# Optimization experiments

Hardware: AMD Instinct MI355X
Metric: run time of the kernel (lower is better)

## Reference

```python
import jax, jax.numpy as jnp
import numpy as np


def setup_inputs() -> dict:
    key = jax.random.key(0)
    k1, k2 = jax.random.split(key)
    N, K, E = 65536, 8, 64  # tokens, top_k, num_experts
    top_scores = jax.random.normal(k1, (N, K), dtype=jnp.float32)
    selected_experts_indices = jax.random.randint(k2, (N, K), 0, E, dtype=jnp.int32)
    return {
        "top_scores": top_scores,
        "selected_experts_indices": selected_experts_indices,
        "num_experts": E,
        "top_k": K,
    }


def reference(top_scores, selected_experts_indices, num_experts, top_k):
    # Flatten (token, slot) assignments: total = N * top_k
    expert_flat = selected_experts_indices.reshape(-1)

    # Histogram: number of assignments per expert (float32, matching torch impl)
    num_tokens_per_expert = jax.ops.segment_sum(
        jnp.ones_like(expert_flat, dtype=jnp.float32),
        expert_flat,
        num_segments=num_experts,
    )

    # Stable sort by expert id == counting sort: for each output slot, which
    # flattened assignment index lands there. Identical to the torch
    # scatter/cumsum counting-sort since both are stable.
    token_indices_experts_sorted = jnp.argsort(expert_flat, stable=True)

    # Gather routing scores into expert-sorted order
    top_scores_experts_sorted = top_scores.reshape(-1)[token_indices_experts_sorted]

    # Map flattened assignment index back to token index
    token_indices_experts_sorted = token_indices_experts_sorted // top_k

    return (top_scores_experts_sorted, token_indices_experts_sorted, num_tokens_per_expert)
```

## Files before the change

### kernel.cpp

```cpp
#include <hip/hip_runtime.h>

#define TOTAL   524288
#define NEXP    64
#define TOPK    8
#define GSIZE   256
#define BLOCK   256
#define NWAVE   4
#define CHUNK   (TOTAL / GSIZE)
#define WCHUNK  (CHUNK / NWAVE)
#define WROUNDS (WCHUNK / 64)

__global__ __launch_bounds__(BLOCK) void hist_kernel(const int* __restrict__ idx,
                                                     int* __restrict__ counts) {
    __shared__ int hist[NWAVE][NEXP];
    const int tid = threadIdx.x, lane = tid & 63, wave = tid >> 6;
    hist[wave][lane] = 0;
    const int base = blockIdx.x * CHUNK + wave * WCHUNK;
#pragma unroll
    for (int r = 0; r < WROUNDS; r++) {
        const int e = idx[base + r * 64 + lane];
        unsigned long long m = ~0ULL;
#pragma unroll
        for (int bit = 0; bit < 6; bit++) {
            const unsigned long long bb = __ballot((e >> bit) & 1);
            m &= ((e >> bit) & 1) ? bb : ~bb;
        }
        const int leader = __ffsll((long long)m) - 1;
        if (lane == leader) hist[wave][e] += __popcll(m);
    }
    __syncthreads();
    if (tid < NEXP)
        counts[blockIdx.x * NEXP + tid] =
            hist[0][tid] + hist[1][tid] + hist[2][tid] + hist[3][tid];
}

__global__ __launch_bounds__(BLOCK) void scatter_kernel(
        const float* __restrict__ scores,
        const int*   __restrict__ idx,
        const int*   __restrict__ counts,
        float*       __restrict__ out_scores,
        float*       __restrict__ out_tok,
        float*       __restrict__ out_cnt) {
    __shared__ int hist[NWAVE][NEXP];
    __shared__ int part_pre[NWAVE][NEXP];
    __shared__ int part_tot[NWAVE][NEXP];
    __shared__ int exscan_pre[NEXP];
    __shared__ int exoff[NWAVE][NEXP];
    __shared__ int run[NWAVE][NEXP];

    const int tid = threadIdx.x, lane = tid & 63, wave = tid >> 6, b = blockIdx.x;
    const unsigned long long ltmask = (1ULL << lane) - 1ULL;

    int pre = 0, tot = 0;
    {
        const int bb0 = wave * (GSIZE / NWAVE);
#pragma unroll 16
        for (int q = 0; q < GSIZE / NWAVE; q++) {
            const int bb = bb0 + q;
            const int c  = counts[bb * NEXP + lane];
            tot += c;
            pre += (bb < b) ? c : 0;
        }
    }
    part_pre[wave][lane] = pre;
    part_tot[wave][lane] = tot;

    hist[wave][lane] = 0;
    run[wave][lane]  = 0;
    const int base = b * CHUNK + wave * WCHUNK;
    int                myE[WROUNDS];
    float              myS[WROUNDS];
    unsigned long long myM[WROUNDS];
#pragma unroll
    for (int r = 0; r < WROUNDS; r++) {
        const int i = base + r * 64 + lane;
        const int e = idx[i];
        myE[r] = e;
        myS[r] = scores[i];
        unsigned long long m = ~0ULL;
#pragma unroll
        for (int bit = 0; bit < 6; bit++) {
            const unsigned long long bb = __ballot((e >> bit) & 1);
            m &= ((e >> bit) & 1) ? bb : ~bb;
        }
        myM[r] = m;
        const int leader = __ffsll((long long)m) - 1;
        if (lane == leader) hist[wave][e] += __popcll(m);
    }
    __syncthreads();

    if (wave == 0) {
        const int p = part_pre[0][lane] + part_pre[1][lane] +
                      part_pre[2][lane] + part_pre[3][lane];
        const int t = part_tot[0][lane] + part_tot[1][lane] +
                      part_tot[2][lane] + part_tot[3][lane];
        if (b == 0) out_cnt[lane] = (float)t;
        int inc = t;
#pragma unroll
        for (int d = 1; d < 64; d <<= 1) {
            const int v = __shfl_up(inc, d, 64);
            if (lane >= d) inc += v;
        }
        exscan_pre[lane] = (inc - t) + p;
    }
    __syncthreads();

    {
        int off = exscan_pre[lane];
        for (int w = 0; w < wave; w++) off += hist[w][lane];
        exoff[wave][lane] = off;
    }
    __syncthreads();

#pragma unroll
    for (int r = 0; r < WROUNDS; r++) {
        const int e = myE[r];
        const unsigned long long m = myM[r];
        const int inwave = __popcll(m & ltmask);
        const int rn     = run[wave][e];
        const int pos    = exoff[wave][e] + rn + inwave;
        out_scores[pos] = myS[r];
        out_tok[pos]    = (float)((base + r * 64 + lane) >> 3);
        __builtin_amdgcn_wave_barrier();
        const int leader = __ffsll((long long)m) - 1;
        if (lane == leader) run[wave][e] = rn + __popcll(m);
        __builtin_amdgcn_wave_barrier();
    }
}

extern "C" void kernel_launch(void* const* d_in, const int* in_sizes, int n_in,
                              void* d_out, int out_size, void* d_ws, size_t ws_size,
                              hipStream_t stream) {
    const float* top_scores = (const float*)d_in[0];
    const int*   sel_idx    = (const int*)d_in[1];
    float*       out        = (float*)d_out;
    int*         counts     = (int*)d_ws;

    float* out_scores = out;
    float* out_tok    = out + TOTAL;
    float* out_cnt    = out + 2 * TOTAL;

    hist_kernel<<<GSIZE, BLOCK, 0, stream>>>(sel_idx, counts);
    scatter_kernel<<<GSIZE, BLOCK, 0, stream>>>(top_scores, sel_idx, counts,
                                                out_scores, out_tok, out_cnt);
}
```

Measured before the change: 73.84 us.

## Use 1024-thread blocks with two elements per thread and shuffle-based ranking

Both kernels now use 1024-thread blocks of 16 waves, and each thread loads one int2/float2 pair instead of looping over several rounds per wave. Per-expert counts are computed per lane from six ballots, which removes the leader-based LDS read-modify-write. In the scatter, each element's rank comes from shuffling the per-expert masks and wave bases, which removes the serial running-offset loop and its wave barriers. The cost is more waves per block to combine in the prefix step, and each wave's 64-row counts scan covers fewer rows but spreads across more waves.

New measurement: 67.43 us. 1.1x faster.

```diff
diff --git a/kernel.cpp b/kernel.cpp
--- a/kernel.cpp
+++ b/kernel.cpp
@@ -4,34 +4,43 @@
 #define NEXP    64
 #define TOPK    8
 #define GSIZE   256
-#define BLOCK   256
-#define NWAVE   4
+#define BLOCK   1024
+#define NWAVE   16
 #define CHUNK   (TOTAL / GSIZE)
 #define WCHUNK  (CHUNK / NWAVE)
-#define WROUNDS (WCHUNK / 64)
+#define ROWSPW  (GSIZE / NWAVE)
+
+__device__ __forceinline__ unsigned long long expert_mask(
+        const unsigned long long bb[6], int x) {
+    unsigned long long m = ~0ULL;
+#pragma unroll
+    for (int bit = 0; bit < 6; bit++)
+        m &= ((x >> bit) & 1) ? bb[bit] : ~bb[bit];
+    return m;
+}
 
 __global__ __launch_bounds__(BLOCK) void hist_kernel(const int* __restrict__ idx,
                                                      int* __restrict__ counts) {
     __shared__ int hist[NWAVE][NEXP];
     const int tid = threadIdx.x, lane = tid & 63, wave = tid >> 6;
-    hist[wave][lane] = 0;
-    const int base = blockIdx.x * CHUNK + wave * WCHUNK;
+
+    const int2 e2 = ((const int2*)idx)[blockIdx.x * (CHUNK / 2) + tid];
+
+    unsigned long long bb0[6], bb1[6];
 #pragma unroll
-    for (int r = 0; r < WROUNDS; r++) {
-        const int e = idx[base + r * 64 + lane];
-        unsigned long long m = ~0ULL;
+    for (int bit = 0; bit < 6; bit++) {
+        bb0[bit] = __ballot((e2.x >> bit) & 1);
+        bb1[bit] = __ballot((e2.y >> bit) & 1);
+    }
+    hist[wave][lane] = __popcll(expert_mask(bb0, lane)) +
+                       __popcll(expert_mask(bb1, lane));
+    __syncthreads();
+    if (tid < NEXP) {
+        int s = 0;
 #pragma unroll
-        for (int bit = 0; bit < 6; bit++) {
-            const unsigned long long bb = __ballot((e >> bit) & 1);
-            m &= ((e >> bit) & 1) ? bb : ~bb;
-        }
-        const int leader = __ffsll((long long)m) - 1;
-        if (lane == leader) hist[wave][e] += __popcll(m);
+        for (int w = 0; w < NWAVE; w++) s += hist[w][tid];
+        counts[blockIdx.x * NEXP + tid] = s;
     }
-    __syncthreads();
-    if (tid < NEXP)
-        counts[blockIdx.x * NEXP + tid] =
-            hist[0][tid] + hist[1][tid] + hist[2][tid] + hist[3][tid];
 }
 
 __global__ __launch_bounds__(BLOCK) void scatter_kernel(
@@ -41,22 +50,24 @@
         float*       __restrict__ out_scores,
         float*       __restrict__ out_tok,
         float*       __restrict__ out_cnt) {
-    __shared__ int hist[NWAVE][NEXP];
     __shared__ int part_pre[NWAVE][NEXP];
     __shared__ int part_tot[NWAVE][NEXP];
+    __shared__ int wtot[NWAVE][NEXP];
     __shared__ int exscan_pre[NEXP];
-    __shared__ int exoff[NWAVE][NEXP];
-    __shared__ int run[NWAVE][NEXP];
 
     const int tid = threadIdx.x, lane = tid & 63, wave = tid >> 6, b = blockIdx.x;
-    const unsigned long long ltmask = (1ULL << lane) - 1ULL;
+    const unsigned long long lt  = (1ULL << lane) - 1ULL;
+    const unsigned long long own = 1ULL << lane;
+
+    const int2   e2 = ((const int2*)idx)[b * (CHUNK / 2) + tid];
+    const float2 s2 = ((const float2*)scores)[b * (CHUNK / 2) + tid];
 
     int pre = 0, tot = 0;
     {
-        const int bb0 = wave * (GSIZE / NWAVE);
-#pragma unroll 16
-        for (int q = 0; q < GSIZE / NWAVE; q++) {
-            const int bb = bb0 + q;
+        const int r0 = wave * ROWSPW;
+#pragma unroll
+        for (int q = 0; q < ROWSPW; q++) {
+            const int bb = r0 + q;
             const int c  = counts[bb * NEXP + lane];
             tot += c;
             pre += (bb < b) ? c : 0;
@@ -65,35 +76,25 @@
     part_pre[wave][lane] = pre;
     part_tot[wave][lane] = tot;
 
-    hist[wave][lane] = 0;
-    run[wave][lane]  = 0;
-    const int base = b * CHUNK + wave * WCHUNK;
-    int                myE[WROUNDS];
-    float              myS[WROUNDS];
-    unsigned long long myM[WROUNDS];
+    const int e0 = e2.x, e1 = e2.y;
+    unsigned long long bb0[6], bb1[6];
 #pragma unroll
-    for (int r = 0; r < WROUNDS; r++) {
-        const int i = base + r * 64 + lane;
-        const int e = idx[i];
-        myE[r] = e;
-        myS[r] = scores[i];
-        unsigned long long m = ~0ULL;
-#pragma unroll
-        for (int bit = 0; bit < 6; bit++) {
-            const unsigned long long bb = __ballot((e >> bit) & 1);
-            m &= ((e >> bit) & 1) ? bb : ~bb;
-        }
-        myM[r] = m;
-        const int leader = __ffsll((long long)m) - 1;
-        if (lane == leader) hist[wave][e] += __popcll(m);
+    for (int bit = 0; bit < 6; bit++) {
+        bb0[bit] = __ballot((e0 >> bit) & 1);
+        bb1[bit] = __ballot((e1 >> bit) & 1);
     }
+    const unsigned long long M0 = expert_mask(bb0, lane);
+    const unsigned long long M1 = expert_mask(bb1, lane);
+    wtot[wave][lane] = __popcll(M0) + __popcll(M1);
     __syncthreads();
 
     if (wave == 0) {
-        const int p = part_pre[0][lane] + part_pre[1][lane] +
-                      part_pre[2][lane] + part_pre[3][lane];
-        const int t = part_tot[0][lane] + part_tot[1][lane] +
-                      part_tot[2][lane] + part_tot[3][lane];
+        int p = 0, t = 0;
+#pragma unroll
+        for (int w = 0; w < NWAVE; w++) {
+            p += part_pre[w][lane];
+            t += part_tot[w][lane];
+        }
         if (b == 0) out_cnt[lane] = (float)t;
         int inc = t;
 #pragma unroll
@@ -105,27 +106,29 @@
     }
     __syncthreads();
 
-    {
-        int off = exscan_pre[lane];
-        for (int w = 0; w < wave; w++) off += hist[w][lane];
-        exoff[wave][lane] = off;
-    }
-    __syncthreads();
+    int base = exscan_pre[lane];
+#pragma unroll
+    for (int w = 0; w < NWAVE; w++)
+        base += (w < wave) ? wtot[w][lane] : 0;
 
-#pragma unroll
-    for (int r = 0; r < WROUNDS; r++) {
-        const int e = myE[r];
-        const unsigned long long m = myM[r];
-        const int inwave = __popcll(m & ltmask);
-        const int rn     = run[wave][e];
-        const int pos    = exoff[wave][e] + rn + inwave;
-        out_scores[pos] = myS[r];
-        out_tok[pos]    = (float)((base + r * 64 + lane) >> 3);
-        __builtin_amdgcn_wave_barrier();
-        const int leader = __ffsll((long long)m) - 1;
-        if (lane == leader) run[wave][e] = rn + __popcll(m);
-        __builtin_amdgcn_wave_barrier();
-    }
+    const unsigned long long own0 = __shfl(M0, e0, 64);
+    const unsigned long long own1 = __shfl(M1, e1, 64);
+    const unsigned long long c01  = __shfl(M1, e0, 64);
+    const unsigned long long c10  = __shfl(M0, e1, 64);
+    const int base0 = __shfl(base, e0, 64);
+    const int base1 = __shfl(base, e1, 64);
+
+    const int rank0 = __popcll(own0 & lt) + __popcll(c01 & lt);
+    const int rank1 = __popcll(c10 & (lt | own)) + __popcll(own1 & lt);
+
+    const int f0 = b * CHUNK + 2 * tid;
+    const int pos0 = base0 + rank0;
+    const int pos1 = base1 + rank1;
+
+    out_scores[pos0] = s2.x;
+    out_scores[pos1] = s2.y;
+    out_tok[pos0]    = (float)(f0 >> 3);
+    out_tok[pos1]    = (float)((f0 + 1) >> 3);
 }
 
 extern "C" void kernel_launch(void* const* d_in, const int* in_sizes, int n_in,
```
